# Performance work log

Hardware: AMD Instinct MI355X
Metric: run time of the kernel (lower is better)

## Reference

```python
import jax, jax.numpy as jnp
import numpy as np

B, T, D, H = 4, 2048, 1024, 16
HS = D // H
EPS = 1e-5

def layer_norm(x, g, b):
    mu = jnp.mean(x, axis=-1, keepdims=True)
    var = jnp.var(x, axis=-1, keepdims=True)
    return (x - mu) * jax.lax.rsqrt(var + EPS) * g + b

def setup_inputs() -> dict:
    key = jax.random.key(0)
    ks = jax.random.split(key, 12)
    s_in = 1.0 / np.sqrt(D)
    s_ff = 1.0 / np.sqrt(4 * D)
    return {
        "x": jax.random.normal(ks[0], (B, T, D), jnp.float32),
        "Wq": jax.random.uniform(ks[1], (H, D, HS), jnp.float32, -s_in, s_in),
        "Wk": jax.random.uniform(ks[2], (H, D, HS), jnp.float32, -s_in, s_in),
        "Wv": jax.random.uniform(ks[3], (H, D, HS), jnp.float32, -s_in, s_in),
        "Wp": jax.random.uniform(ks[4], (D, D), jnp.float32, -s_in, s_in),
        "bp": jax.random.uniform(ks[5], (D,), jnp.float32, -s_in, s_in),
        "W1": jax.random.uniform(ks[6], (D, 4 * D), jnp.float32, -s_in, s_in),
        "b1": jax.random.uniform(ks[7], (4 * D,), jnp.float32, -s_in, s_in),
        "W2": jax.random.uniform(ks[8], (4 * D, D), jnp.float32, -s_ff, s_ff),
        "b2": jax.random.uniform(ks[9], (D,), jnp.float32, -s_ff, s_ff),
        "g1": jnp.ones((D,), jnp.float32),
        "be1": jnp.zeros((D,), jnp.float32),
        "g2": jnp.ones((D,), jnp.float32),
        "be2": jnp.zeros((D,), jnp.float32),
    }

def reference(x, Wq, Wk, Wv, Wp, bp, W1, b1, W2, b2, g1, be1, g2, be2):
    # pre-LN (note: residual uses the NORMALIZED tensor, matching original code)
    h = layer_norm(x, g1, be1)                          # [B,T,D]
    q = jnp.einsum('btd,hdk->bhtk', h, Wq)              # [B,H,T,hs]
    k = jnp.einsum('btd,hdk->bhtk', h, Wk)
    v = jnp.einsum('btd,hdk->bhtk', h, Wv)
    # NOTE: original scales by embedding_size**-0.5, not head_size
    scores = jnp.einsum('bhtk,bhsk->bhts', q, k) * (D ** -0.5)
    causal = jnp.tril(jnp.ones((T, T), bool))
    scores = jnp.where(causal, scores, -jnp.inf)
    att = jax.nn.softmax(scores, axis=-1)               # [B,H,T,T]
    o = jnp.einsum('bhts,bhsk->bhtk', att, v)
    o = o.transpose(0, 2, 1, 3).reshape(B, T, D)        # concat heads
    o = o @ Wp + bp
    x2 = h + o
    h2 = layer_norm(x2, g2, be2)
    ff = jax.nn.relu(h2 @ W1 + b1) @ W2 + b2
    return h2 + ff
```

## Files before the change

kernel.cpp:

```cpp
#include <hip/hip_runtime.h>
#include <hip/hip_bf16.h>

#define Bq 4
#define Tq 2048
#define Dq 1024
#define Hq 16
#define HSq 64
#define EPSq 1e-5f

typedef __attribute__((ext_vector_type(8))) short s16x8;
typedef __attribute__((ext_vector_type(4))) float f32x4;

#define GLL16(g, l)                                                        \
    __builtin_amdgcn_global_load_lds(                                      \
        (const __attribute__((address_space(1))) void*)(g),                \
        (__attribute__((address_space(3))) void*)(l), 16, 0, 0)

#define PH_BAR() do { __builtin_amdgcn_sched_barrier(0);                   \
                      __builtin_amdgcn_s_barrier();                        \
                      __builtin_amdgcn_sched_barrier(0); } while (0)

__device__ __forceinline__ ushort f2bf(float f) {
    union { float f; unsigned u; } x; x.f = f;
    unsigned r = x.u + 0x7fffu + ((x.u >> 16) & 1u);
    return (ushort)(r >> 16);
}

__global__ __launch_bounds__(256) void ln_bf16(const float* __restrict__ x,
                                               const float* __restrict__ g,
                                               const float* __restrict__ bb,
                                               float* __restrict__ y,
                                               ushort* __restrict__ y16) {
    __shared__ float sdata[8];
    int row = blockIdx.x;
    const float4* xr = (const float4*)(x + (size_t)row * Dq);
    float4 v = xr[threadIdx.x];
    float s  = v.x + v.y + v.z + v.w;
    float ss = v.x*v.x + v.y*v.y + v.z*v.z + v.w*v.w;
    for (int off = 32; off; off >>= 1) {
        s  += __shfl_down(s,  off);
        ss += __shfl_down(ss, off);
    }
    int lane = threadIdx.x & 63, wid = threadIdx.x >> 6;
    if (lane == 0) { sdata[wid] = s; sdata[4 + wid] = ss; }
    __syncthreads();
    if (threadIdx.x == 0) {
        sdata[0] = sdata[0] + sdata[1] + sdata[2] + sdata[3];
        sdata[4] = sdata[4] + sdata[5] + sdata[6] + sdata[7];
    }
    __syncthreads();
    float mu  = sdata[0] * (1.f / Dq);
    float var = sdata[4] * (1.f / Dq) - mu * mu;
    float inv = rsqrtf(var + EPSq);
    float4 gv = ((const float4*)g)[threadIdx.x];
    float4 bv = ((const float4*)bb)[threadIdx.x];
    float4 o;
    o.x = (v.x - mu) * inv * gv.x + bv.x;
    o.y = (v.y - mu) * inv * gv.y + bv.y;
    o.z = (v.z - mu) * inv * gv.z + bv.z;
    o.w = (v.w - mu) * inv * gv.w + bv.w;
    ((float4*)(y + (size_t)row * Dq))[threadIdx.x] = o;
    ushort4 u4;
    u4.x = f2bf(o.x); u4.y = f2bf(o.y); u4.z = f2bf(o.z); u4.w = f2bf(o.w);
    *(ushort4*)(y16 + (size_t)row * Dq + threadIdx.x * 4) = u4;
}

__global__ __launch_bounds__(256) void repack_qkvT(const float* __restrict__ Wqm,
                                                   const float* __restrict__ Wkm,
                                                   const float* __restrict__ Wvm,
                                                   ushort* __restrict__ out) {
    __shared__ float tile[64][65];
    int bid = blockIdx.x;
    int p  = bid >> 8;
    int hh = (bid >> 4) & 15;
    int kt = bid & 15;
    int k0 = kt * 64;
    const float* W = (p == 0) ? Wqm : ((p == 1) ? Wkm : Wvm);
    float scale = (p == 0) ? 0.03125f : 1.0f;
    int j  = threadIdx.x & 63;
    int i0 = threadIdx.x >> 6;
#pragma unroll
    for (int r = 0; r < 16; r++) {
        int i = r * 4 + i0;
        tile[i][j] = W[(size_t)hh * (Dq * HSq) + (size_t)(k0 + i) * HSq + j];
    }
    __syncthreads();
#pragma unroll
    for (int r = 0; r < 16; r++) {
        int i = r * 4 + i0;
        out[(size_t)(p * Dq + hh * HSq + i) * Dq + k0 + j] = f2bf(tile[j][i] * scale);
    }
}

__global__ __launch_bounds__(256) void transpose_cvt(const float* __restrict__ in,
                                                     ushort* __restrict__ out,
                                                     int K, int N) {
    __shared__ float tile[64][65];
    int k0 = blockIdx.y * 64, n0 = blockIdx.x * 64;
    int j  = threadIdx.x & 63;
    int i0 = threadIdx.x >> 6;
#pragma unroll
    for (int r = 0; r < 16; r++) {
        int i = r * 4 + i0;
        tile[i][j] = in[(size_t)(k0 + i) * N + n0 + j];
    }
    __syncthreads();
#pragma unroll
    for (int r = 0; r < 16; r++) {
        int i = r * 4 + i0;
        out[(size_t)(n0 + i) * K + k0 + j] = f2bf(tile[j][i]);
    }
}

__global__ __launch_bounds__(256, 2) void gemm_bf16(const ushort* __restrict__ A,
                                                    const ushort* __restrict__ BT,
                                                    const float* __restrict__ bias,
                                                    const float* __restrict__ resid,
                                                    void* __restrict__ Cp,
                                                    ushort* __restrict__ vtg,
                                                    int M, int N, int K,
                                                    int lda, int ldc,
                                                    int relu, int out_bf16) {
    __shared__ ushort lds[2 * 8192 + 3 * 8192];
    ushort* Alds = lds;
    ushort* Blds = lds + 2 * 8192;

    int tid = threadIdx.x;
    int w = tid >> 6, lane = tid & 63;
    int lm = lane & 15, quad = lane >> 4;
    int wm = w >> 1, wn = w & 1;

    int nwg = gridDim.x;
    int bid = blockIdx.x;
    int wk = bid;
    if ((nwg & 7) == 0) { int cpx = nwg >> 3; wk = (bid & 7) * cpx + (bid >> 3); }
    int mtiles = M >> 7;
    int rt = wk % mtiles, ct = wk / mtiles;
    int row0 = rt << 7, col0 = ct << 7;

    int cswz = (lane & 7) ^ (lane >> 3);
    int srow = w * 8 + (lane >> 3);
    const ushort* pA = A  + (size_t)(row0 + srow) * lda + cswz * 8;
    const ushort* pB = BT + (size_t)(col0 + srow) * K  + cswz * 8;

    auto stageA = [&](int slot, int t) {
#pragma unroll
        for (int s = 0; s < 4; s++)
            GLL16(pA + (size_t)t * 64 + (size_t)(s * 32) * lda,
                  Alds + slot * 8192 + s * 2048 + w * 512);
    };
    auto stageB = [&](int slot, int t) {
#pragma unroll
        for (int s = 0; s < 4; s++)
            GLL16(pB + (size_t)t * 64 + (size_t)(s * 32) * K,
                  Blds + slot * 8192 + s * 2048 + w * 512);
    };

    int swq0 = (quad * 8) ^ ((lm & 7) << 3);
    int swq1 = (32 + quad * 8) ^ ((lm & 7) << 3);

    f32x4 zero = {0.f, 0.f, 0.f, 0.f};
    f32x4 acc[4][4];
#pragma unroll
    for (int i = 0; i < 4; i++)
#pragma unroll
        for (int jj = 0; jj < 4; jj++) acc[i][jj] = zero;

    int nkt = K >> 6;

    stageA(0, 0);
    stageB(0, 0);
    stageB(1, 1);
    __builtin_amdgcn_sched_barrier(0);
    asm volatile("s_waitcnt vmcnt(4)" ::: "memory");
    __builtin_amdgcn_s_barrier();
    __builtin_amdgcn_sched_barrier(0);

    int sA = 0, sB = 0;
    for (int t = 0; t < nkt; ++t) {
        const bool stA = (t + 1 < nkt);
        const bool stB = (t + 2 < nkt);
        int sB2 = sB + 2; if (sB2 >= 3) sB2 -= 3;
        const ushort* Ab = Alds + sA * 8192 + (wm * 64 + lm) * 64;
        const ushort* Bb = Blds + sB * 8192 + (wn * 64 + lm) * 64;
        s16x8 a[4][2], b0[2][2], b1[2][2];

#pragma unroll
        for (int m = 0; m < 4; m++) {
            a[m][0] = *(const s16x8*)(Ab + m * 1024 + swq0);
            a[m][1] = *(const s16x8*)(Ab + m * 1024 + swq1);
        }
#pragma unroll
        for (int nf = 0; nf < 2; nf++) {
            b0[nf][0] = *(const s16x8*)(Bb + nf * 1024 + swq0);
            b0[nf][1] = *(const s16x8*)(Bb + nf * 1024 + swq1);
        }
        if (stA) stageA(sA ^ 1, t + 1);
        PH_BAR();
        __builtin_amdgcn_s_setprio(1);
#pragma unroll
        for (int m = 0; m < 4; m++)
#pragma unroll
            for (int nf = 0; nf < 2; nf++) {
                f32x4 tt = __builtin_amdgcn_mfma_f32_16x16x32_bf16(a[m][0], b0[nf][0], acc[m][nf], 0, 0, 0);
                acc[m][nf] = __builtin_amdgcn_mfma_f32_16x16x32_bf16(a[m][1], b0[nf][1], tt, 0, 0, 0);
            }
        __builtin_amdgcn_s_setprio(0);
        PH_BAR();

#pragma unroll
        for (int nf = 0; nf < 2; nf++) {
            b1[nf][0] = *(const s16x8*)(Bb + (nf + 2) * 1024 + swq0);
            b1[nf][1] = *(const s16x8*)(Bb + (nf + 2) * 1024 + swq1);
        }
        if (stB) stageB(sB2, t + 2);
        PH_BAR();
        __builtin_amdgcn_s_setprio(1);
#pragma unroll
        for (int m = 0; m < 4; m++)
#pragma unroll
            for (int nf = 0; nf < 2; nf++) {
                f32x4 tt = __builtin_amdgcn_mfma_f32_16x16x32_bf16(a[m][0], b1[nf][0], acc[m][nf + 2], 0, 0, 0);
                acc[m][nf + 2] = __builtin_amdgcn_mfma_f32_16x16x32_bf16(a[m][1], b1[nf][1], tt, 0, 0, 0);
            }
        __builtin_amdgcn_s_setprio(0);
        __builtin_amdgcn_sched_barrier(0);
        if (stB)      { asm volatile("s_waitcnt vmcnt(4)" ::: "memory"); }
        else if (stA) { asm volatile("s_waitcnt vmcnt(0)" ::: "memory"); }
        if (stA) {
            __builtin_amdgcn_s_barrier();
            __builtin_amdgcn_sched_barrier(0);
        }

        sA ^= 1;
        sB += 1; if (sB >= 3) sB -= 3;
    }

    if (vtg && col0 >= 2048) {
#pragma unroll
        for (int m = 0; m < 4; m++) {
            int r0 = row0 + wm * 64 + m * 16 + quad * 4;
            int bb = r0 >> 11;
            int t  = r0 & (Tq - 1);
#pragma unroll
            for (int nf = 0; nf < 4; nf++) {
                int hsg = col0 - 2048 + wn * 64 + nf * 16 + lm;
                ushort4 u;
                u.x = f2bf(acc[m][nf][0]);
                u.y = f2bf(acc[m][nf][1]);
                u.z = f2bf(acc[m][nf][2]);
                u.w = f2bf(acc[m][nf][3]);
                *(ushort4*)(vtg + ((size_t)(bb * Hq + (hsg >> 6)) * HSq + (hsg & 63)) * Tq + t) = u;
            }
        }
        return;
    }

    float bcol[4];
#pragma unroll
    for (int nf = 0; nf < 4; nf++)
        bcol[nf] = bias ? bias[col0 + wn * 64 + nf * 16 + lm] : 0.f;

#pragma unroll
    for (int m = 0; m < 4; m++) {
#pragma unroll
        for (int p = 0; p < 4; p++) {
            int r = row0 + wm * 64 + m * 16 + quad * 4 + p;
#pragma unroll
            for (int nf = 0; nf < 4; nf++) {
                int cc = col0 + wn * 64 + nf * 16 + lm;
                float v = acc[m][nf][p] + bcol[nf];
                if (relu) v = fmaxf(v, 0.f);
                if (resid) v += resid[(size_t)r * ldc + cc];
                if (out_bf16) ((ushort*)Cp)[(size_t)r * ldc + cc] = f2bf(v);
                else          ((float*)Cp)[(size_t)r * ldc + cc] = v;
            }
        }
    }
}

__global__ __launch_bounds__(256) void attn_mfma(const ushort* __restrict__ qkv,
                                                 const ushort* __restrict__ VtG,
                                                 ushort* __restrict__ o16) {
    __shared__ ushort Ks[64 * 72];
    __shared__ ushort Vt[64 * 64];
    __shared__ ushort Ps[4 * 16 * 72];

    int gid = blockIdx.x;
    int b  = gid >> 8;
    int hh = (gid >> 4) & 15;
    int pr = (gid + 7 * b) & 15;
    int qa = pr;
    int qb = 31 - pr;

    int tid = threadIdx.x;
    int w = tid >> 6, lane = tid & 63;
    int lm = lane & 15, quad = lane >> 4;

    const int rs3 = 3 * Dq;
    const ushort* qbase = qkv + (size_t)(b * Tq) * rs3 + hh * HSq;
    int qra = qa * 64 + w * 16 + lm;
    int qrb = qb * 64 + w * 16 + lm;
    s16x8 aqa0 = *(const s16x8*)(qbase + (size_t)qra * rs3 + quad * 8);
    s16x8 aqa1 = *(const s16x8*)(qbase + (size_t)qra * rs3 + 32 + quad * 8);
    s16x8 aqb0 = *(const s16x8*)(qbase + (size_t)qrb * rs3 + quad * 8);
    s16x8 aqb1 = *(const s16x8*)(qbase + (size_t)qrb * rs3 + 32 + quad * 8);

    s16x8 ones;
#pragma unroll
    for (int j = 0; j < 8; j++) ones[j] = (short)0x3F80;

    f32x4 zero = {0.f, 0.f, 0.f, 0.f};
    f32x4 oa[4], ob[4];
#pragma unroll
    for (int nt = 0; nt < 4; nt++) { oa[nt] = zero; ob[nt] = zero; }
    f32x4 la = zero, lb = zero;

    const ushort* kbase = qkv + (size_t)(b * Tq) * rs3 + Dq + hh * HSq;
    const ushort* vtb = VtG + (size_t)((b * Hq + hh) * HSq) * Tq;

    int kr = tid >> 3, kc = (tid & 7) * 8;
    int vh = tid >> 2, vc0 = (tid & 3) * 8;
    int vswz = (((vh >> 3) ^ vh) & 7) << 3;

    s16x8 kp0 = *(const s16x8*)(kbase + (size_t)kr * rs3 + kc);
    s16x8 kp1 = *(const s16x8*)(kbase + (size_t)(kr + 32) * rs3 + kc);
    s16x8 vp0 = *(const s16x8*)(vtb + (size_t)vh * Tq + vc0);
    s16x8 vp1 = *(const s16x8*)(vtb + (size_t)vh * Tq + vc0 + 32);

    auto do_tile = [&](const s16x8& aq0, const s16x8& aq1,
                       f32x4 (&o_acc)[4], f32x4& l_acc, int diag) {
        f32x4 sacc[4];
#pragma unroll
        for (int kt2 = 0; kt2 < 4; kt2++) {
            const ushort* krp = &Ks[(kt2 * 16 + lm) * 72 + quad * 8];
            s16x8 bk0 = *(const s16x8*)krp;
            s16x8 bk1 = *(const s16x8*)(krp + 32);
            f32x4 t = __builtin_amdgcn_mfma_f32_16x16x32_bf16(aq0, bk0, zero, 0, 0, 0);
            sacc[kt2] = __builtin_amdgcn_mfma_f32_16x16x32_bf16(aq1, bk1, t, 0, 0, 0);
        }
        if (diag) {
#pragma unroll
            for (int kt2 = 0; kt2 < 4; kt2++)
#pragma unroll
                for (int r = 0; r < 4; r++)
                    if (kt2 * 16 + lm > w * 16 + quad * 4 + r) sacc[kt2][r] = -1e30f;
        }
#pragma unroll
        for (int kt2 = 0; kt2 < 4; kt2++)
#pragma unroll
            for (int r = 0; r < 4; r++)
                Ps[(w * 16 + quad * 4 + r) * 72 + kt2 * 16 + lm] = f2bf(__expf(sacc[kt2][r]));

        s16x8 ap0 = *(const s16x8*)&Ps[(w * 16 + lm) * 72 + quad * 8];
        s16x8 ap1 = *(const s16x8*)&Ps[(w * 16 + lm) * 72 + 32 + quad * 8];

#pragma unroll
        for (int nt = 0; nt < 4; nt++) {
            int n = nt * 16 + lm;
            int swz = (((n >> 3) ^ n) & 7) << 3;
            s16x8 bv0 = *(const s16x8*)&Vt[n * 64 + ((quad * 8) ^ swz)];
            s16x8 bv1 = *(const s16x8*)&Vt[n * 64 + ((32 + quad * 8) ^ swz)];
            f32x4 t = __builtin_amdgcn_mfma_f32_16x16x32_bf16(ap0, bv0, o_acc[nt], 0, 0, 0);
            o_acc[nt] = __builtin_amdgcn_mfma_f32_16x16x32_bf16(ap1, bv1, t, 0, 0, 0);
        }
        f32x4 t2 = __builtin_amdgcn_mfma_f32_16x16x32_bf16(ap0, ones, l_acc, 0, 0, 0);
        l_acc = __builtin_amdgcn_mfma_f32_16x16x32_bf16(ap1, ones, t2, 0, 0, 0);
    };

    for (int kt = 0; kt <= qb; kt++) {
        __syncthreads();
        *(s16x8*)&Ks[kr * 72 + kc] = kp0;
        *(s16x8*)&Ks[(kr + 32) * 72 + kc] = kp1;
        *(s16x8*)&Vt[vh * 64 + (vc0 ^ vswz)] = vp0;
        *(s16x8*)&Vt[vh * 64 + ((vc0 + 32) ^ vswz)] = vp1;
        __syncthreads();

        if (kt < qb) {
            const ushort* kb = kbase + (size_t)((kt + 1) * 64) * rs3;
            kp0 = *(const s16x8*)(kb + (size_t)kr * rs3 + kc);
            kp1 = *(const s16x8*)(kb + (size_t)(kr + 32) * rs3 + kc);
            const ushort* vb = vtb + (size_t)vh * Tq + (kt + 1) * 64;
            vp0 = *(const s16x8*)(vb + vc0);
            vp1 = *(const s16x8*)(vb + vc0 + 32);
        }

        do_tile(aqb0, aqb1, ob, lb, kt == qb);
        if (kt <= qa)
            do_tile(aqa0, aqa1, oa, la, kt == qa);
    }

#pragma unroll
    for (int r = 0; r < 4; r++) {
        float inva = 1.f / la[r];
        float invb = 1.f / lb[r];
        size_t rowa = (size_t)(b * Tq + qa * 64 + w * 16 + quad * 4 + r);
        size_t rowb = (size_t)(b * Tq + qb * 64 + w * 16 + quad * 4 + r);
#pragma unroll
        for (int nt = 0; nt < 4; nt++) {
            o16[rowa * Dq + hh * HSq + nt * 16 + lm] = f2bf(oa[nt][r] * inva);
            o16[rowb * Dq + hh * HSq + nt * 16 + lm] = f2bf(ob[nt][r] * invb);
        }
    }
}

extern "C" void kernel_launch(void* const* d_in, const int* in_sizes, int n_in,
                              void* d_out, int out_size, void* d_ws, size_t ws_size,
                              hipStream_t stream) {
    const float* x   = (const float*)d_in[0];
    const float* Wq  = (const float*)d_in[1];
    const float* Wk  = (const float*)d_in[2];
    const float* Wv  = (const float*)d_in[3];
    const float* Wp  = (const float*)d_in[4];
    const float* bp  = (const float*)d_in[5];
    const float* W1  = (const float*)d_in[6];
    const float* b1  = (const float*)d_in[7];
    const float* W2  = (const float*)d_in[8];
    const float* b2  = (const float*)d_in[9];
    const float* g1  = (const float*)d_in[10];
    const float* be1 = (const float*)d_in[11];
    const float* g2  = (const float*)d_in[12];
    const float* be2 = (const float*)d_in[13];
    float* out = (float*)d_out;

    const size_t MB = 1u << 20;
    char* ws = (char*)d_ws;
    float*  slotA = (float*)(ws);
    ushort* qkv   = (ushort*)(ws + 32 * MB);
    float*  pbuf  = (float*)(ws + 32 * MB);
    ushort* u16   = (ushort*)(ws + 32 * MB);
    ushort* slotC = (ushort*)(ws + 96 * MB);
    ushort* WqkvT = (ushort*)(ws + 112 * MB);
    ushort* WpT   = (ushort*)(ws + 118 * MB);
    ushort* W1T   = (ushort*)(ws + 120 * MB);
    ushort* W2T   = (ushort*)(ws + 128 * MB);
    ushort* VtG   = (ushort*)(ws + 136 * MB);

    const int rows = Bq * Tq;

    hipLaunchKernelGGL(repack_qkvT, dim3(3 * 16 * 16), dim3(256), 0, stream, Wq, Wk, Wv, WqkvT);
    hipLaunchKernelGGL(transpose_cvt, dim3(Dq / 64, Dq / 64), dim3(256), 0, stream, Wp, WpT, Dq, Dq);
    hipLaunchKernelGGL(transpose_cvt, dim3(4 * Dq / 64, Dq / 64), dim3(256), 0, stream, W1, W1T, Dq, 4 * Dq);
    hipLaunchKernelGGL(transpose_cvt, dim3(Dq / 64, 4 * Dq / 64), dim3(256), 0, stream, W2, W2T, 4 * Dq, Dq);

    hipLaunchKernelGGL(ln_bf16, dim3(rows), dim3(256), 0, stream, x, g1, be1, slotA, slotC);
    hipLaunchKernelGGL(gemm_bf16, dim3((rows / 128) * (3 * Dq / 128)), dim3(256), 0, stream,
                       slotC, WqkvT, (const float*)nullptr, (const float*)nullptr, (void*)qkv, VtG,
                       rows, 3 * Dq, Dq, Dq, 3 * Dq, 0, 1);
    hipLaunchKernelGGL(attn_mfma, dim3(Bq * Hq * 16), dim3(256), 0, stream, qkv, VtG, slotC);
    hipLaunchKernelGGL(gemm_bf16, dim3((rows / 128) * (Dq / 128)), dim3(256), 0, stream,
                       slotC, WpT, bp, slotA, (void*)pbuf, (ushort*)nullptr,
                       rows, Dq, Dq, Dq, Dq, 0, 0);
    hipLaunchKernelGGL(ln_bf16, dim3(rows), dim3(256), 0, stream, pbuf, g2, be2, slotA, slotC);
    hipLaunchKernelGGL(gemm_bf16, dim3((rows / 128) * (4 * Dq / 128)), dim3(256), 0, stream,
                       slotC, W1T, b1, (const float*)nullptr, (void*)u16, (ushort*)nullptr,
                       rows, 4 * Dq, Dq, Dq, 4 * Dq, 1, 1);
    hipLaunchKernelGGL(gemm_bf16, dim3((rows / 128) * (Dq / 128)), dim3(256), 0, stream,
                       u16, W2T, b2, slotA, (void*)out, (ushort*)nullptr,
                       rows, Dq, 4 * Dq, 4 * Dq, Dq, 0, 0);
}
```

Baseline: 544.8 us.

## Halve GEMM K-tile to 32, shrink LDS, raise occupancy and remap tiles per XCD

The bf16 GEMM's K step drops from 64 to 32, which halves LDS use per block and removes the XOR swizzle in favour of a plain 4-chunk row layout. Launch bounds go from 2 to 4 blocks per CU. A new tile-to-block mapping gives each XCD a contiguous band of 8 row tiles and walks column tiles in super-rows of width sr, aiming for better L2 reuse. The risks are LDS bank conflicts from the unswizzled layout, twice as many barriers per unit of K, and register pressure under the tighter launch bounds.

```diff
diff --git a/kernel.cpp b/kernel.cpp
--- a/kernel.cpp
+++ b/kernel.cpp
@@ -112,7 +112,7 @@
     }
 }
 
-__global__ __launch_bounds__(256, 2) void gemm_bf16(const ushort* __restrict__ A,
+__global__ __launch_bounds__(256, 4) void gemm_bf16(const ushort* __restrict__ A,
                                                     const ushort* __restrict__ BT,
                                                     const float* __restrict__ bias,
                                                     const float* __restrict__ resid,
@@ -120,44 +120,45 @@
                                                     ushort* __restrict__ vtg,
                                                     int M, int N, int K,
                                                     int lda, int ldc,
-                                                    int relu, int out_bf16) {
-    __shared__ ushort lds[2 * 8192 + 3 * 8192];
+                                                    int relu, int out_bf16,
+                                                    int sr) {
+    __shared__ ushort lds[2 * 4096 + 3 * 4096];
     ushort* Alds = lds;
-    ushort* Blds = lds + 2 * 8192;
+    ushort* Blds = lds + 2 * 4096;
 
     int tid = threadIdx.x;
     int w = tid >> 6, lane = tid & 63;
     int lm = lane & 15, quad = lane >> 4;
     int wm = w >> 1, wn = w & 1;
 
-    int nwg = gridDim.x;
     int bid = blockIdx.x;
-    int wk = bid;
-    if ((nwg & 7) == 0) { int cpx = nwg >> 3; wk = (bid & 7) * cpx + (bid >> 3); }
-    int mtiles = M >> 7;
-    int rt = wk % mtiles, ct = wk / mtiles;
+    int mtiles = M >> 7, ntiles = N >> 7;
+    int rt, ct;
+    if (mtiles == 64 && (gridDim.x & 7) == 0) {
+        int xcd = bid & 7, l = bid >> 3;
+        int band = l / (sr * ntiles);
+        int rem  = l - band * sr * ntiles;
+        ct = rem / sr;
+        int srt = rem - ct * sr;
+        rt = xcd * 8 + band * sr + srt;
+    } else {
+        rt = bid % mtiles; ct = bid / mtiles;
+    }
     int row0 = rt << 7, col0 = ct << 7;
 
-    int cswz = (lane & 7) ^ (lane >> 3);
-    int srow = w * 8 + (lane >> 3);
-    const ushort* pA = A  + (size_t)(row0 + srow) * lda + cswz * 8;
-    const ushort* pB = BT + (size_t)(col0 + srow) * K  + cswz * 8;
+    int srow = w * 16 + (lane >> 2);
+    int schk = lane & 3;
+    const ushort* pA = A  + (size_t)(row0 + srow) * lda + schk * 8;
+    const ushort* pB = BT + (size_t)(col0 + srow) * K  + schk * 8;
 
     auto stageA = [&](int slot, int t) {
-#pragma unroll
-        for (int s = 0; s < 4; s++)
-            GLL16(pA + (size_t)t * 64 + (size_t)(s * 32) * lda,
-                  Alds + slot * 8192 + s * 2048 + w * 512);
+        GLL16(pA + (size_t)t * 32, Alds + slot * 4096 + w * 512);
+        GLL16(pA + (size_t)t * 32 + (size_t)64 * lda, Alds + slot * 4096 + 2048 + w * 512);
     };
     auto stageB = [&](int slot, int t) {
-#pragma unroll
-        for (int s = 0; s < 4; s++)
-            GLL16(pB + (size_t)t * 64 + (size_t)(s * 32) * K,
-                  Blds + slot * 8192 + s * 2048 + w * 512);
+        GLL16(pB + (size_t)t * 32, Blds + slot * 4096 + w * 512);
+        GLL16(pB + (size_t)t * 32 + (size_t)64 * K, Blds + slot * 4096 + 2048 + w * 512);
     };
-
-    int swq0 = (quad * 8) ^ ((lm & 7) << 3);
-    int swq1 = (32 + quad * 8) ^ ((lm & 7) << 3);
 
     f32x4 zero = {0.f, 0.f, 0.f, 0.f};
     f32x4 acc[4][4];
@@ -166,13 +167,13 @@
 #pragma unroll
         for (int jj = 0; jj < 4; jj++) acc[i][jj] = zero;
 
-    int nkt = K >> 6;
+    int nkt = K >> 5;
 
     stageA(0, 0);
     stageB(0, 0);
     stageB(1, 1);
     __builtin_amdgcn_sched_barrier(0);
-    asm volatile("s_waitcnt vmcnt(4)" ::: "memory");
+    asm volatile("s_waitcnt vmcnt(2)" ::: "memory");
     __builtin_amdgcn_s_barrier();
     __builtin_amdgcn_sched_barrier(0);
 
@@ -181,51 +182,41 @@
         const bool stA = (t + 1 < nkt);
         const bool stB = (t + 2 < nkt);
         int sB2 = sB + 2; if (sB2 >= 3) sB2 -= 3;
-        const ushort* Ab = Alds + sA * 8192 + (wm * 64 + lm) * 64;
-        const ushort* Bb = Blds + sB * 8192 + (wn * 64 + lm) * 64;
-        s16x8 a[4][2], b0[2][2], b1[2][2];
-
-#pragma unroll
-        for (int m = 0; m < 4; m++) {
-            a[m][0] = *(const s16x8*)(Ab + m * 1024 + swq0);
-            a[m][1] = *(const s16x8*)(Ab + m * 1024 + swq1);
-        }
-#pragma unroll
-        for (int nf = 0; nf < 2; nf++) {
-            b0[nf][0] = *(const s16x8*)(Bb + nf * 1024 + swq0);
-            b0[nf][1] = *(const s16x8*)(Bb + nf * 1024 + swq1);
-        }
+        const ushort* Ab = Alds + sA * 4096 + (wm * 64 + lm) * 32;
+        const ushort* Bb = Blds + sB * 4096 + (wn * 64 + lm) * 32;
+        s16x8 a[4], b0[2], b1[2];
+
+#pragma unroll
+        for (int m = 0; m < 4; m++)
+            a[m] = *(const s16x8*)(Ab + m * 512 + quad * 8);
+#pragma unroll
+        for (int nf = 0; nf < 2; nf++)
+            b0[nf] = *(const s16x8*)(Bb + nf * 512 + quad * 8);
         if (stA) stageA(sA ^ 1, t + 1);
         PH_BAR();
         __builtin_amdgcn_s_setprio(1);
 #pragma unroll
         for (int m = 0; m < 4; m++)
 #pragma unroll
-            for (int nf = 0; nf < 2; nf++) {
-                f32x4 tt = __builtin_amdgcn_mfma_f32_16x16x32_bf16(a[m][0], b0[nf][0], acc[m][nf], 0, 0, 0);
-                acc[m][nf] = __builtin_amdgcn_mfma_f32_16x16x32_bf16(a[m][1], b0[nf][1], tt, 0, 0, 0);
-            }
+            for (int nf = 0; nf < 2; nf++)
+                acc[m][nf] = __builtin_amdgcn_mfma_f32_16x16x32_bf16(a[m], b0[nf], acc[m][nf], 0, 0, 0);
         __builtin_amdgcn_s_setprio(0);
         PH_BAR();
 
 #pragma unroll
-        for (int nf = 0; nf < 2; nf++) {
-            b1[nf][0] = *(const s16x8*)(Bb + (nf + 2) * 1024 + swq0);
-            b1[nf][1] = *(const s16x8*)(Bb + (nf + 2) * 1024 + swq1);
-        }
+        for (int nf = 0; nf < 2; nf++)
+            b1[nf] = *(const s16x8*)(Bb + (nf + 2) * 512 + quad * 8);
         if (stB) stageB(sB2, t + 2);
         PH_BAR();
         __builtin_amdgcn_s_setprio(1);
 #pragma unroll
         for (int m = 0; m < 4; m++)
 #pragma unroll
-            for (int nf = 0; nf < 2; nf++) {
-                f32x4 tt = __builtin_amdgcn_mfma_f32_16x16x32_bf16(a[m][0], b1[nf][0], acc[m][nf + 2], 0, 0, 0);
-                acc[m][nf + 2] = __builtin_amdgcn_mfma_f32_16x16x32_bf16(a[m][1], b1[nf][1], tt, 0, 0, 0);
-            }
+            for (int nf = 0; nf < 2; nf++)
+                acc[m][nf + 2] = __builtin_amdgcn_mfma_f32_16x16x32_bf16(a[m], b1[nf], acc[m][nf + 2], 0, 0, 0);
         __builtin_amdgcn_s_setprio(0);
         __builtin_amdgcn_sched_barrier(0);
-        if (stB)      { asm volatile("s_waitcnt vmcnt(4)" ::: "memory"); }
+        if (stB)      { asm volatile("s_waitcnt vmcnt(2)" ::: "memory"); }
         else if (stA) { asm volatile("s_waitcnt vmcnt(0)" ::: "memory"); }
         if (stA) {
             __builtin_amdgcn_s_barrier();
@@ -446,16 +437,16 @@
     hipLaunchKernelGGL(ln_bf16, dim3(rows), dim3(256), 0, stream, x, g1, be1, slotA, slotC);
     hipLaunchKernelGGL(gemm_bf16, dim3((rows / 128) * (3 * Dq / 128)), dim3(256), 0, stream,
                        slotC, WqkvT, (const float*)nullptr, (const float*)nullptr, (void*)qkv, VtG,
-                       rows, 3 * Dq, Dq, Dq, 3 * Dq, 0, 1);
+                       rows, 3 * Dq, Dq, Dq, 3 * Dq, 0, 1, 8);
     hipLaunchKernelGGL(attn_mfma, dim3(Bq * Hq * 16), dim3(256), 0, stream, qkv, VtG, slotC);
     hipLaunchKernelGGL(gemm_bf16, dim3((rows / 128) * (Dq / 128)), dim3(256), 0, stream,
                        slotC, WpT, bp, slotA, (void*)pbuf, (ushort*)nullptr,
-                       rows, Dq, Dq, Dq, Dq, 0, 0);
+                       rows, Dq, Dq, Dq, Dq, 0, 0, 8);
     hipLaunchKernelGGL(ln_bf16, dim3(rows), dim3(256), 0, stream, pbuf, g2, be2, slotA, slotC);
     hipLaunchKernelGGL(gemm_bf16, dim3((rows / 128) * (4 * Dq / 128)), dim3(256), 0, stream,
                        slotC, W1T, b1, (const float*)nullptr, (void*)u16, (ushort*)nullptr,
-                       rows, 4 * Dq, Dq, Dq, 4 * Dq, 1, 1);
+                       rows, 4 * Dq, Dq, Dq, 4 * Dq, 1, 1, 8);
     hipLaunchKernelGGL(gemm_bf16, dim3((rows / 128) * (Dq / 128)), dim3(256), 0, stream,
                        u16, W2T, b2, slotA, (void*)out, (ushort*)nullptr,
-                       rows, Dq, 4 * Dq, 4 * Dq, Dq, 0, 0);
-}
+                       rows, Dq, 4 * Dq, 4 * Dq, Dq, 0, 0, 4);
+}
```

After: 515.8 us. -5.3%, faster.
